# Kernel optimization log

Hardware: AMD Instinct MI355X
Metric: run time of the kernel (lower is better)

Reference implementation:

```python
import jax, jax.numpy as jnp
import numpy as np

N, D = 4096, 512
NUM_CLASSES = 100


def setup_inputs() -> dict:
    key = jax.random.key(0)
    k1, k2, k3 = jax.random.split(key, 3)
    image_features = jax.random.normal(k1, (N, D), dtype=jnp.float32)
    text_features = jax.random.normal(k2, (N, D), dtype=jnp.float32)
    labels = jax.random.randint(k3, (N,), 0, NUM_CLASSES, dtype=jnp.int64)
    return {
        "image_features": image_features,
        "text_features": text_features,
        "labels": labels,
    }


def reference(image_features, text_features, labels):
    # mask[i,j] = 1 if labels[i] != labels[j] else 0 (vectorized O(N^2) loops)
    mask = (labels[:, None] != labels[None, :]).astype(image_features.dtype)  # [N,N]

    # L2-normalize along feature dim (F.normalize, p=2, dim=1)
    img = image_features / jnp.linalg.norm(image_features, axis=1, keepdims=True)
    txt = text_features / jnp.linalg.norm(text_features, axis=1, keepdims=True)

    # neg_similarity = sum(exp((txt @ img.T) @ mask))  -- faithful to source
    sim = txt @ img.T                      # [N,N]
    neg_similarity = jnp.sum(jnp.exp(sim @ mask))

    # pos_sim_i = exp(<img_i, txt_i>); loss_i = log(pos / (pos + neg))
    pos_sim = jnp.exp(jnp.sum(img * txt, axis=1))  # [N]
    pos_log = jnp.log(pos_sim / (pos_sim + neg_similarity))
    return -jnp.sum(pos_log)
```

## Files before the change

kernel.cpp:

```cpp
#include <hip/hip_runtime.h>

#define NN 4096
#define DD 512
#define CP 128
#define MT 64
#define NB2 (NN / MT)

#define NEG_OFF   0
#define DONE_OFF  1
#define D_OFF     64
#define INVI_OFF  (64 + NN)
#define INVT_OFF  (64 + 2*NN)
#define CNTF_OFF  (64 + 3*NN)
#define TXB_OFF_W 16384
#define GB_OFF_W  (TXB_OFF_W + NN*DD/2)

typedef __attribute__((ext_vector_type(8))) short bf16x8;
typedef __attribute__((ext_vector_type(4))) float f32x4;

static __device__ inline unsigned short f2bf(float f) {
    unsigned int u = __float_as_uint(f);
    unsigned int r = u + 0x7fffu + ((u >> 16) & 1u);
    return (unsigned short)(r >> 16);
}

__global__ __launch_bounds__(256) void k1_rows(const float* __restrict__ img,
                                               const float* __restrict__ txt,
                                               float* __restrict__ ws) {
    int w = threadIdx.x >> 6, l = threadIdx.x & 63;
    int row = blockIdx.x * 4 + w;
    const float4* i4 = (const float4*)(img + (size_t)row * DD);
    const float4* t4 = (const float4*)(txt + (size_t)row * DD);
    float4 a0 = i4[l], a1 = i4[l + 64];
    float4 b0 = t4[l], b1 = t4[l + 64];
    float ssi = a0.x*a0.x + a0.y*a0.y + a0.z*a0.z + a0.w*a0.w
              + a1.x*a1.x + a1.y*a1.y + a1.z*a1.z + a1.w*a1.w;
    float sst = b0.x*b0.x + b0.y*b0.y + b0.z*b0.z + b0.w*b0.w
              + b1.x*b1.x + b1.y*b1.y + b1.z*b1.z + b1.w*b1.w;
    float dot = a0.x*b0.x + a0.y*b0.y + a0.z*b0.z + a0.w*b0.w
              + a1.x*b1.x + a1.y*b1.y + a1.z*b1.z + a1.w*b1.w;
    #pragma unroll
    for (int o = 32; o >= 1; o >>= 1) {
        ssi += __shfl_xor(ssi, o);
        sst += __shfl_xor(sst, o);
        dot += __shfl_xor(dot, o);
    }
    float inv_t = rsqrtf(sst);
    unsigned short* txb = (unsigned short*)(ws + TXB_OFF_W);
    ushort4 s0, s1;
    s0.x = f2bf(b0.x * inv_t); s0.y = f2bf(b0.y * inv_t);
    s0.z = f2bf(b0.z * inv_t); s0.w = f2bf(b0.w * inv_t);
    s1.x = f2bf(b1.x * inv_t); s1.y = f2bf(b1.y * inv_t);
    s1.z = f2bf(b1.z * inv_t); s1.w = f2bf(b1.w * inv_t);
    *(ushort4*)(txb + (size_t)row * DD + 4 * l)       = s0;
    *(ushort4*)(txb + (size_t)row * DD + 256 + 4 * l) = s1;
    if (l == 0) {
        float inv_i = rsqrtf(ssi);
        ws[D_OFF + row]    = dot * inv_i * inv_t;
        ws[INVI_OFF + row] = inv_i;
        ws[INVT_OFF + row] = inv_t;
    }
    if (blockIdx.x == 0 && threadIdx.x == 0) {
        ws[NEG_OFF] = 0.0f;
        ((int*)ws)[DONE_OFF] = 0;
    }
}

__global__ __launch_bounds__(512) void k1b_gather(const float* __restrict__ img,
                                                  const int* __restrict__ labels,
                                                  float* __restrict__ ws) {
    __shared__ int list[256];
    __shared__ int scnt;
    __shared__ float4 pg[4][128];
    int c = blockIdx.x;
    int t = threadIdx.x;
    if (t < 64) {
        int cnt = 0;
        for (int i = 0; i < NN / 64; ++i) {
            int lab = labels[i * 64 + t];
            unsigned long long m = __ballot(lab == c);
            int pre = (int)__popcll(m & ((1ull << t) - 1ull));
            if (lab == c) {
                int p = cnt + pre;
                if (p < 256) list[p] = i * 64 + t;
            }
            cnt += (int)__popcll(m);
        }
        if (t == 0) scnt = cnt < 256 ? cnt : 256;
    }
    __syncthreads();
    int n   = scnt;
    int sub = t >> 7;
    int l   = t & 127;
    const float* invi  = ws + INVI_OFF;
    const float4* img4 = (const float4*)img;
    float ax = 0.f, ay = 0.f, az = 0.f, aw = 0.f;
    for (int s = sub; s < n; s += 4) {
        int j = list[s];
        float wv = invi[j];
        float4 v = img4[(size_t)j * 128 + l];
        ax += v.x * wv; ay += v.y * wv; az += v.z * wv; aw += v.w * wv;
    }
    float4 mine; mine.x = ax; mine.y = ay; mine.z = az; mine.w = aw;
    pg[sub][l] = mine;
    __syncthreads();
    if (sub == 0) {
        float4 r0 = pg[0][l], r1 = pg[1][l], r2 = pg[2][l], r3 = pg[3][l];
        float rx = r0.x + r1.x + r2.x + r3.x;
        float ry = r0.y + r1.y + r2.y + r3.y;
        float rz = r0.z + r1.z + r2.z + r3.z;
        float rw = r0.w + r1.w + r2.w + r3.w;
        unsigned short* gbf = (unsigned short*)(ws + GB_OFF_W);
        ushort4 o;
        o.x = f2bf(rx); o.y = f2bf(ry); o.z = f2bf(rz); o.w = f2bf(rw);
        *(ushort4*)(gbf + (size_t)c * DD + 4 * l) = o;
        if (l == 0) ws[CNTF_OFF + c] = (float)n;
    }
}

__global__ __launch_bounds__(256) void k2_neg(float* __restrict__ ws,
                                              float* __restrict__ out) {
    __shared__ __align__(16) unsigned short As[2][MT * 32];
    __shared__ __align__(16) unsigned short Bs[2][CP * 32];
    __shared__ float cnts[CP];
    __shared__ float wred[4];
    __shared__ float sneg;
    __shared__ int   sdone;
    int t = threadIdx.x;
    int w = t >> 6, l = t & 63;
    int row0 = blockIdx.x * MT;
    if (t < CP) cnts[t] = ws[CNTF_OFF + t];
    const unsigned short* txb = (const unsigned short*)(ws + TXB_OFF_W);
    const unsigned short* gbf = (const unsigned short*)(ws + GB_OFF_W);

    int arow = t >> 2, koct = t & 3;
    const int4* gA  = (const int4*)(txb + (size_t)(row0 + arow) * DD + koct * 8);
    const int4* gB0 = (const int4*)(gbf + (size_t)arow * DD + koct * 8);
    const int4* gB1 = (const int4*)(gbf + (size_t)(arow + 64) * DD + koct * 8);
    unsigned short* wA  = &As[0][arow * 32 + koct * 8];
    unsigned short* wB0 = &Bs[0][arow * 32 + koct * 8];
    unsigned short* wB1 = &Bs[0][(arow + 64) * 32 + koct * 8];

    f32x4 acc[8];
    f32x4 zero = {0.f, 0.f, 0.f, 0.f};
    #pragma unroll
    for (int f = 0; f < 8; ++f) acc[f] = zero;

    int4 ra = gA[0], rb0 = gB0[0], rb1 = gB1[0];
    *(int4*)wA = ra; *(int4*)wB0 = rb0; *(int4*)wB1 = rb1;
    __syncthreads();

    int afoff = (w * 16 + (l & 15)) * 32 + (l >> 4) * 8;
    int bfoff = (l & 15) * 32 + (l >> 4) * 8;

    for (int ch = 0; ch < 16; ++ch) {
        int cur = ch & 1;
        if (ch < 15) {
            ra  = gA [(ch + 1) * 4];
            rb0 = gB0[(ch + 1) * 4];
            rb1 = gB1[(ch + 1) * 4];
        }
        bf16x8 af = *(const bf16x8*)&As[cur][afoff];
        #pragma unroll
        for (int f = 0; f < 8; ++f) {
            bf16x8 bfr = *(const bf16x8*)&Bs[cur][f * 16 * 32 + bfoff];
            acc[f] = __builtin_amdgcn_mfma_f32_16x16x32_bf16(af, bfr, acc[f], 0, 0, 0);
        }
        if (ch < 15) {
            int nxt = cur ^ 1;
            *(int4*)(wA  + nxt * MT * 32) = ra;
            *(int4*)(wB0 + nxt * CP * 32) = rb0;
            *(int4*)(wB1 + nxt * CP * 32) = rb1;
        }
        __syncthreads();
    }

    float rs[4];
    #pragma unroll
    for (int r = 0; r < 4; ++r) {
        float s = 0.f;
        #pragma unroll
        for (int f = 0; f < 8; ++f) s += acc[f][r];
        #pragma unroll
        for (int o = 1; o < 16; o <<= 1) s += __shfl_xor(s, o);
        rs[r] = s;
    }
    float p = 0.f;
    #pragma unroll
    for (int f = 0; f < 8; ++f) {
        float cf = cnts[f * 16 + (l & 15)];
        float e = 0.f;
        #pragma unroll
        for (int r = 0; r < 4; ++r) e += __expf(rs[r] - acc[f][r]);
        p += cf * e;
    }
    #pragma unroll
    for (int o = 32; o >= 1; o >>= 1) p += __shfl_xor(p, o);
    if (l == 0) wred[w] = p;
    __syncthreads();
    if (t == 0) {
        atomicAdd(ws + NEG_OFF, wred[0] + wred[1] + wred[2] + wred[3]);
        __threadfence();
        int old = atomicAdd((int*)ws + DONE_OFF, 1);
        sdone = (old == NB2 - 1);
        if (sdone) sneg = atomicAdd(ws + NEG_OFF, 0.0f);
    }
    __syncthreads();
    if (sdone) {
        float neg = sneg;
        float s = 0.f;
        for (int i = t; i < NN; i += 256) {
            float dv = ws[D_OFF + i];
            s += logf(__expf(dv) + neg) - dv;
        }
        #pragma unroll
        for (int o = 32; o >= 1; o >>= 1) s += __shfl_xor(s, o);
        __syncthreads();
        if (l == 0) wred[w] = s;
        __syncthreads();
        if (t == 0) out[0] = wred[0] + wred[1] + wred[2] + wred[3];
    }
}

extern "C" void kernel_launch(void* const* d_in, const int* in_sizes, int n_in,
                              void* d_out, int out_size, void* d_ws, size_t ws_size,
                              hipStream_t stream) {
    const float* img  = (const float*)d_in[0];
    const float* txt  = (const float*)d_in[1];
    const int* labels = (const int*)d_in[2];
    float* ws  = (float*)d_ws;
    float* out = (float*)d_out;

    k1_rows<<<NN / 4, 256, 0, stream>>>(img, txt, ws);
    k1b_gather<<<CP, 512, 0, stream>>>(img, labels, ws);
    k2_neg<<<NB2, 256, 0, stream>>>(ws, out);
}
```

Before: 104.8 us.

## Split k2 into 16-row tiles with class-split waves and swizzled LDS

The similarity-by-class-sum kernel now handles 16 text rows per block instead of 64, so it launches four times as many blocks. Each block stages the full 16-row A tile and half of the class-sum matrix in XOR-swizzled shared memory, in two K halves. The four waves now split the 128 classes among themselves rather than splitting rows. Row sums are combined across waves through shared memory. The aim is to fill far more compute units and cut LDS bank conflicts, at the cost of reloading the class-sum matrix from global memory in every block and using much more shared memory per block.

```diff
diff --git a/kernel.cpp b/kernel.cpp
--- a/kernel.cpp
+++ b/kernel.cpp
@@ -3,7 +3,7 @@
 #define NN 4096
 #define DD 512
 #define CP 128
-#define MT 64
+#define MT 16
 #define NB2 (NN / MT)
 
 #define NEG_OFF   0
@@ -120,9 +120,11 @@
 
 __global__ __launch_bounds__(256) void k2_neg(float* __restrict__ ws,
                                               float* __restrict__ out) {
-    __shared__ __align__(16) unsigned short As[2][MT * 32];
-    __shared__ __align__(16) unsigned short Bs[2][CP * 32];
+    __shared__ __align__(16) unsigned char As[MT * DD * 2];
+    __shared__ __align__(16) unsigned char Bs[CP * 256 * 2];
     __shared__ float cnts[CP];
+    __shared__ float part[4][MT];
+    __shared__ float Ss[MT];
     __shared__ float wred[4];
     __shared__ float sneg;
     __shared__ int   sdone;
@@ -131,67 +133,94 @@
     int row0 = blockIdx.x * MT;
     if (t < CP) cnts[t] = ws[CNTF_OFF + t];
     const unsigned short* txb = (const unsigned short*)(ws + TXB_OFF_W);
-    const unsigned short* gbf = (const unsigned short*)(ws + GB_OFF_W);
-
-    int arow = t >> 2, koct = t & 3;
-    const int4* gA  = (const int4*)(txb + (size_t)(row0 + arow) * DD + koct * 8);
-    const int4* gB0 = (const int4*)(gbf + (size_t)arow * DD + koct * 8);
-    const int4* gB1 = (const int4*)(gbf + (size_t)(arow + 64) * DD + koct * 8);
-    unsigned short* wA  = &As[0][arow * 32 + koct * 8];
-    unsigned short* wB0 = &Bs[0][arow * 32 + koct * 8];
-    unsigned short* wB1 = &Bs[0][(arow + 64) * 32 + koct * 8];
-
-    f32x4 acc[8];
-    f32x4 zero = {0.f, 0.f, 0.f, 0.f};
-    #pragma unroll
-    for (int f = 0; f < 8; ++f) acc[f] = zero;
-
-    int4 ra = gA[0], rb0 = gB0[0], rb1 = gB1[0];
-    *(int4*)wA = ra; *(int4*)wB0 = rb0; *(int4*)wB1 = rb1;
-    __syncthreads();
-
-    int afoff = (w * 16 + (l & 15)) * 32 + (l >> 4) * 8;
-    int bfoff = (l & 15) * 32 + (l >> 4) * 8;
-
-    for (int ch = 0; ch < 16; ++ch) {
-        int cur = ch & 1;
-        if (ch < 15) {
-            ra  = gA [(ch + 1) * 4];
-            rb0 = gB0[(ch + 1) * 4];
-            rb1 = gB1[(ch + 1) * 4];
-        }
-        bf16x8 af = *(const bf16x8*)&As[cur][afoff];
-        #pragma unroll
-        for (int f = 0; f < 8; ++f) {
-            bf16x8 bfr = *(const bf16x8*)&Bs[cur][f * 16 * 32 + bfoff];
-            acc[f] = __builtin_amdgcn_mfma_f32_16x16x32_bf16(af, bfr, acc[f], 0, 0, 0);
-        }
-        if (ch < 15) {
-            int nxt = cur ^ 1;
-            *(int4*)(wA  + nxt * MT * 32) = ra;
-            *(int4*)(wB0 + nxt * CP * 32) = rb0;
-            *(int4*)(wB1 + nxt * CP * 32) = rb1;
-        }
-        __syncthreads();
-    }
-
-    float rs[4];
+    const int4* gB = (const int4*)(ws + GB_OFF_W);
+    const int4* gA = (const int4*)(txb + (size_t)row0 * DD);
+
+    int ao = t & 63;
+    int bo = t & 31;
+    int4 a0 = gA[((t >> 6) + 0)  * 64 + ao];
+    int4 a1 = gA[((t >> 6) + 4)  * 64 + ao];
+    int4 a2 = gA[((t >> 6) + 8)  * 64 + ao];
+    int4 a3 = gA[((t >> 6) + 12) * 64 + ao];
+    int4 br[16];
+    #pragma unroll
+    for (int s = 0; s < 16; ++s)
+        br[s] = gB[((t >> 5) + 8 * s) * 64 + bo];
+    {
+        int r;
+        r = (t >> 6) + 0;  *(int4*)&As[r * 1024 + ((ao * 16) ^ ((r & 7) << 4))] = a0;
+        r = (t >> 6) + 4;  *(int4*)&As[r * 1024 + ((ao * 16) ^ ((r & 7) << 4))] = a1;
+        r = (t >> 6) + 8;  *(int4*)&As[r * 1024 + ((ao * 16) ^ ((r & 7) << 4))] = a2;
+        r = (t >> 6) + 12; *(int4*)&As[r * 1024 + ((ao * 16) ^ ((r & 7) << 4))] = a3;
+    }
+    #pragma unroll
+    for (int s = 0; s < 16; ++s) {
+        int c = (t >> 5) + 8 * s;
+        *(int4*)&Bs[c * 512 + ((bo * 16) ^ ((c & 7) << 4))] = br[s];
+    }
+    __syncthreads();
+    #pragma unroll
+    for (int s = 0; s < 16; ++s)
+        br[s] = gB[((t >> 5) + 8 * s) * 64 + 32 + bo];
+
+    f32x4 acc[2];
+    acc[0] = (f32x4){0.f, 0.f, 0.f, 0.f};
+    acc[1] = (f32x4){0.f, 0.f, 0.f, 0.f};
+    int arow = l & 15, kq = l >> 4;
+    int c0 = 32 * w;
+    int aswz = (arow & 7) << 4;
+    int cA = c0 + arow, cB = c0 + 16 + arow;
+    int aoffA = cA * 512, aswzA = (cA & 7) << 4;
+    int aoffB = cB * 512, aswzB = (cB & 7) << 4;
+
+    #pragma unroll
+    for (int ch = 0; ch < 8; ++ch) {
+        int kb = ch * 64 + kq * 16;
+        bf16x8 af = *(const bf16x8*)&As[arow * 1024 + (kb ^ aswz)];
+        bf16x8 b0 = *(const bf16x8*)&Bs[aoffA + (kb ^ aswzA)];
+        bf16x8 b1 = *(const bf16x8*)&Bs[aoffB + (kb ^ aswzB)];
+        acc[0] = __builtin_amdgcn_mfma_f32_16x16x32_bf16(af, b0, acc[0], 0, 0, 0);
+        acc[1] = __builtin_amdgcn_mfma_f32_16x16x32_bf16(af, b1, acc[1], 0, 0, 0);
+    }
+    __syncthreads();
+    #pragma unroll
+    for (int s = 0; s < 16; ++s) {
+        int c = (t >> 5) + 8 * s;
+        *(int4*)&Bs[c * 512 + ((bo * 16) ^ ((c & 7) << 4))] = br[s];
+    }
+    __syncthreads();
+    #pragma unroll
+    for (int ch = 0; ch < 8; ++ch) {
+        int kb = ch * 64 + kq * 16;
+        bf16x8 af = *(const bf16x8*)&As[arow * 1024 + ((512 + kb) ^ aswz)];
+        bf16x8 b0 = *(const bf16x8*)&Bs[aoffA + (kb ^ aswzA)];
+        bf16x8 b1 = *(const bf16x8*)&Bs[aoffB + (kb ^ aswzB)];
+        acc[0] = __builtin_amdgcn_mfma_f32_16x16x32_bf16(af, b0, acc[0], 0, 0, 0);
+        acc[1] = __builtin_amdgcn_mfma_f32_16x16x32_bf16(af, b1, acc[1], 0, 0, 0);
+    }
+
+    float rsum[4];
     #pragma unroll
     for (int r = 0; r < 4; ++r) {
-        float s = 0.f;
-        #pragma unroll
-        for (int f = 0; f < 8; ++f) s += acc[f][r];
+        float s = acc[0][r] + acc[1][r];
         #pragma unroll
         for (int o = 1; o < 16; o <<= 1) s += __shfl_xor(s, o);
-        rs[r] = s;
-    }
+        rsum[r] = s;
+    }
+    if ((l & 15) == 0) {
+        #pragma unroll
+        for (int r = 0; r < 4; ++r) part[w][kq * 4 + r] = rsum[r];
+    }
+    __syncthreads();
+    if (t < MT) Ss[t] = part[0][t] + part[1][t] + part[2][t] + part[3][t];
+    __syncthreads();
     float p = 0.f;
     #pragma unroll
-    for (int f = 0; f < 8; ++f) {
-        float cf = cnts[f * 16 + (l & 15)];
+    for (int f = 0; f < 2; ++f) {
+        float cf = cnts[c0 + f * 16 + (l & 15)];
         float e = 0.f;
         #pragma unroll
-        for (int r = 0; r < 4; ++r) e += __expf(rs[r] - acc[f][r]);
+        for (int r = 0; r < 4; ++r) e += __expf(Ss[kq * 4 + r] - acc[f][r]);
         p += cf * e;
     }
     #pragma unroll
```

Measured after the change: 119.2 us. 1.14x slower.
